# Optimization experiments

Measured on AMD Instinct MI355X. Metric: run time of the kernel, lower is better.

Reference implementation:

```python
import jax, jax.numpy as jnp
import numpy as np


def make_base_grid(D, H, W, dtype):
    # torch.affine_grid(align_corners=True) base coords: last dim is (x, y, z)
    # where x varies along W, y along H, z along D, each in [-1, 1].
    zs = jnp.linspace(-1.0, 1.0, D, dtype=dtype)
    ys = jnp.linspace(-1.0, 1.0, H, dtype=dtype)
    xs = jnp.linspace(-1.0, 1.0, W, dtype=dtype)
    gz, gy, gx = jnp.meshgrid(zs, ys, xs, indexing='ij')  # each (D,H,W)
    return jnp.stack([gx, gy, gz], axis=-1)  # (D,H,W,3)


def trilinear_sample(vol, grid):
    # vol: (C,D,H,W); grid: (D,H,W,3) normalized coords (x,y,z);
    # align_corners=True, padding_mode='zeros' (torch grid_sample defaults).
    C, D, H, W = vol.shape
    ix = (grid[..., 0] + 1.0) * 0.5 * (W - 1)
    iy = (grid[..., 1] + 1.0) * 0.5 * (H - 1)
    iz = (grid[..., 2] + 1.0) * 0.5 * (D - 1)
    ix0f, iy0f, iz0f = jnp.floor(ix), jnp.floor(iy), jnp.floor(iz)
    wx, wy, wz = ix - ix0f, iy - iy0f, iz - iz0f
    ix0, iy0, iz0 = ix0f.astype(jnp.int32), iy0f.astype(jnp.int32), iz0f.astype(jnp.int32)
    ix1, iy1, iz1 = ix0 + 1, iy0 + 1, iz0 + 1

    def corner(zi, yi, xi, w):
        valid = ((zi >= 0) & (zi < D) & (yi >= 0) & (yi < H) & (xi >= 0) & (xi < W))
        zc = jnp.clip(zi, 0, D - 1)
        yc = jnp.clip(yi, 0, H - 1)
        xc = jnp.clip(xi, 0, W - 1)
        v = vol[:, zc, yc, xc]  # (C,D,H,W)
        return v * (w * valid.astype(vol.dtype))[None]

    one = jnp.asarray(1.0, vol.dtype)
    out = (corner(iz0, iy0, ix0, (one - wz) * (one - wy) * (one - wx))
           + corner(iz0, iy0, ix1, (one - wz) * (one - wy) * wx)
           + corner(iz0, iy1, ix0, (one - wz) * wy * (one - wx))
           + corner(iz0, iy1, ix1, (one - wz) * wy * wx)
           + corner(iz1, iy0, ix0, wz * (one - wy) * (one - wx))
           + corner(iz1, iy0, ix1, wz * (one - wy) * wx)
           + corner(iz1, iy1, ix0, wz * wy * (one - wx))
           + corner(iz1, iy1, ix1, wz * wy * wx))
    return out  # (C,D,H,W)


def setup_inputs() -> dict:
    key = jax.random.key(0)
    kx, ky = jax.random.split(key)
    shape = (1, 1, 192, 192, 192)
    x = jax.random.uniform(kx, shape, dtype=jnp.float32)
    y = jax.random.uniform(ky, shape, dtype=jnp.float32)
    return {"x": x, "y": y}


def reference(x, y):
    N, C, D, H, W = x.shape
    base = make_base_grid(D, H, W, x.dtype)  # (D,H,W,3) == identity affine_grid
    xv = x[:, 0]  # (N,D,H,W), channel 0 only as in the torch code
    yv = y[:, 0]
    x_sum = jnp.sum(x)
    y_sum = jnp.sum(y)
    # weighted center of mass for each normalized coordinate (x,y,z)
    cm_x = jnp.einsum('ndhw,dhwk->k', xv, base) / x_sum  # (3,)
    cm_y = jnp.einsum('ndhw,dhwk->k', yv, base) / y_sum  # (3,)
    t = cm_x - cm_y  # translation placed in theta[:, :, 3]
    grid = base + t  # (D,H,W,3): affine_grid with identity + translation
    grid_b = jnp.broadcast_to(grid[None], (N, D, H, W, 3))
    transformed = jax.vmap(trilinear_sample)(x, grid_b)  # (N,C,D,H,W)
    return transformed, grid_b
```

## Files before the change

### kernel.cpp

```cpp
#include <hip/hip_runtime.h>
#include <math.h>

#define DD 192
#define HH 192
#define WW 192
#define NVOX (DD*HH*WW)
#define NV4  (NVOX/4)
#define RB   1024
#define RT   256

__device__ __forceinline__ float gcoord(int i, int n) {
    return -1.0f + (float)i * (2.0f / (float)(n - 1));
}

__global__ void reduce_kernel(const float* __restrict__ x,
                              const float* __restrict__ y,
                              double* __restrict__ partials) {
    double acc[8] = {0,0,0,0,0,0,0,0};
    int tid = blockIdx.x * blockDim.x + threadIdx.x;
    const float4* x4 = (const float4*)x;
    const float4* y4 = (const float4*)y;
    for (int i = tid; i < NV4; i += RB * RT) {
        float4 xv = x4[i];
        float4 yv = y4[i];
        int base = i * 4;
        int w = base % WW;
        int rem = base / WW;
        int h = rem % HH;
        int d = rem / HH;
        float gy = gcoord(h, HH);
        float gz = gcoord(d, DD);
        float xs[4] = {xv.x, xv.y, xv.z, xv.w};
        float ys[4] = {yv.x, yv.y, yv.z, yv.w};
        #pragma unroll
        for (int k = 0; k < 4; ++k) {
            float gx = gcoord(w + k, WW);
            acc[0] += (double)xs[k];
            acc[1] += (double)(xs[k] * gx);
            acc[2] += (double)(xs[k] * gy);
            acc[3] += (double)(xs[k] * gz);
            acc[4] += (double)ys[k];
            acc[5] += (double)(ys[k] * gx);
            acc[6] += (double)(ys[k] * gy);
            acc[7] += (double)(ys[k] * gz);
        }
    }
    #pragma unroll
    for (int q = 0; q < 8; ++q) {
        double v = acc[q];
        #pragma unroll
        for (int off = 32; off > 0; off >>= 1)
            v += __shfl_down(v, off, 64);
        acc[q] = v;
    }
    __shared__ double lds[4][8];
    int lane = threadIdx.x & 63;
    int wave = threadIdx.x >> 6;
    if (lane == 0) {
        #pragma unroll
        for (int q = 0; q < 8; ++q) lds[wave][q] = acc[q];
    }
    __syncthreads();
    if (threadIdx.x < 8) {
        int q = threadIdx.x;
        double s = lds[0][q] + lds[1][q] + lds[2][q] + lds[3][q];
        partials[q * RB + blockIdx.x] = s;
    }
}

__global__ void finalize_kernel(const double* __restrict__ partials,
                                float* __restrict__ tvec) {
    __shared__ double red[256];
    double sums[8];
    for (int q = 0; q < 8; ++q) {
        double s = 0.0;
        for (int i = threadIdx.x; i < RB; i += 256) s += partials[q * RB + i];
        red[threadIdx.x] = s;
        __syncthreads();
        for (int stride = 128; stride > 0; stride >>= 1) {
            if (threadIdx.x < stride) red[threadIdx.x] += red[threadIdx.x + stride];
            __syncthreads();
        }
        if (threadIdx.x == 0) sums[q] = red[0];
        __syncthreads();
    }
    if (threadIdx.x == 0) {
        double tx = sums[1] / sums[0] - sums[5] / sums[4];
        double ty = sums[2] / sums[0] - sums[6] / sums[4];
        double tz = sums[3] / sums[0] - sums[7] / sums[4];
        tvec[0] = (float)tx;
        tvec[1] = (float)ty;
        tvec[2] = (float)tz;
    }
}

__global__ void main_kernel(const float* __restrict__ x,
                            const float* __restrict__ tvec,
                            float* __restrict__ out_t,
                            float* __restrict__ out_g) {
    int idx = blockIdx.x * blockDim.x + threadIdx.x;
    if (idx >= NVOX) return;
    float tx = tvec[0], ty = tvec[1], tz = tvec[2];
    int w = idx % WW;
    int rem = idx / WW;
    int h = rem % HH;
    int d = rem / HH;
    float gx = gcoord(w, WW) + tx;
    float gy = gcoord(h, HH) + ty;
    float gz = gcoord(d, DD) + tz;
    out_g[3 * idx + 0] = gx;
    out_g[3 * idx + 1] = gy;
    out_g[3 * idx + 2] = gz;
    float ix = (gx + 1.0f) * 0.5f * (float)(WW - 1);
    float iy = (gy + 1.0f) * 0.5f * (float)(HH - 1);
    float iz = (gz + 1.0f) * 0.5f * (float)(DD - 1);
    float fx = floorf(ix), fy = floorf(iy), fz = floorf(iz);
    float wx = ix - fx, wy = iy - fy, wz = iz - fz;
    int ix0 = (int)fx, iy0 = (int)fy, iz0 = (int)fz;
    float acc = 0.0f;
    #pragma unroll
    for (int dz = 0; dz < 2; ++dz) {
        int zi = iz0 + dz;
        if ((unsigned)zi >= (unsigned)DD) continue;
        float wzz = dz ? wz : 1.0f - wz;
        #pragma unroll
        for (int dy = 0; dy < 2; ++dy) {
            int yi = iy0 + dy;
            if ((unsigned)yi >= (unsigned)HH) continue;
            float wyy = dy ? wy : 1.0f - wy;
            #pragma unroll
            for (int dx = 0; dx < 2; ++dx) {
                int xi = ix0 + dx;
                if ((unsigned)xi >= (unsigned)WW) continue;
                float wxx = dx ? wx : 1.0f - wx;
                acc += x[(zi * HH + yi) * WW + xi] * (wzz * wyy * wxx);
            }
        }
    }
    out_t[idx] = acc;
}

extern "C" void kernel_launch(void* const* d_in, const int* in_sizes, int n_in,
                              void* d_out, int out_size, void* d_ws, size_t ws_size,
                              hipStream_t stream) {
    const float* x = (const float*)d_in[0];
    const float* y = (const float*)d_in[1];
    float* out = (float*)d_out;
    float* out_t = out;
    float* out_g = out + NVOX;
    double* partials = (double*)d_ws;
    float* tvec = (float*)((char*)d_ws + 8 * RB * sizeof(double));
    reduce_kernel<<<RB, RT, 0, stream>>>(x, y, partials);
    finalize_kernel<<<1, 256, 0, stream>>>(partials, tvec);
    main_kernel<<<(NVOX + 255) / 256, 256, 0, stream>>>(x, tvec, out_t, out_g);
}
```

Measured before the change: 198.2 us.

## Precompute uniform trilinear weights and offsets; stage grid output through LDS

Since the translation is the same for every voxel, the finalize kernel now computes the integer offsets and the eight trilinear weights once. The main kernel then uses integer index arithmetic plus validity masks in place of per-voxel floor and weight math. The grid output is staged through shared memory and written as coalesced float4 stores instead of strided scalar stores. The finalize reduction switches to wave shuffles. Precomputing the weights in double could differ slightly from the per-voxel float rounding in the reference.

After: 174.7 us. -11.8%, faster.

```diff
diff --git a/kernel.cpp b/kernel.cpp
--- a/kernel.cpp
+++ b/kernel.cpp
@@ -8,6 +8,12 @@
 #define NV4  (NVOX/4)
 #define RB   1024
 #define RT   256
+
+struct Consts {
+    float tx, ty, tz;
+    float wgt[8];
+    int   dx0, dy0, dz0;
+};
 
 __device__ __forceinline__ float gcoord(int i, int n) {
     return -1.0f + (float)i * (2.0f / (float)(n - 1));
@@ -63,80 +69,101 @@
     __syncthreads();
     if (threadIdx.x < 8) {
         int q = threadIdx.x;
-        double s = lds[0][q] + lds[1][q] + lds[2][q] + lds[3][q];
-        partials[q * RB + blockIdx.x] = s;
+        partials[q * RB + blockIdx.x] = lds[0][q] + lds[1][q] + lds[2][q] + lds[3][q];
     }
 }
 
 __global__ void finalize_kernel(const double* __restrict__ partials,
-                                float* __restrict__ tvec) {
-    __shared__ double red[256];
-    double sums[8];
+                                Consts* __restrict__ cs) {
+    double s[8];
+    #pragma unroll
     for (int q = 0; q < 8; ++q) {
-        double s = 0.0;
-        for (int i = threadIdx.x; i < RB; i += 256) s += partials[q * RB + i];
-        red[threadIdx.x] = s;
-        __syncthreads();
-        for (int stride = 128; stride > 0; stride >>= 1) {
-            if (threadIdx.x < stride) red[threadIdx.x] += red[threadIdx.x + stride];
-            __syncthreads();
-        }
-        if (threadIdx.x == 0) sums[q] = red[0];
-        __syncthreads();
+        double v = 0.0;
+        for (int i = threadIdx.x; i < RB; i += 256) v += partials[q * RB + i];
+        #pragma unroll
+        for (int off = 32; off > 0; off >>= 1)
+            v += __shfl_down(v, off, 64);
+        s[q] = v;
     }
+    __shared__ double lds[4][8];
+    int lane = threadIdx.x & 63;
+    int wave = threadIdx.x >> 6;
+    if (lane == 0) {
+        #pragma unroll
+        for (int q = 0; q < 8; ++q) lds[wave][q] = s[q];
+    }
+    __syncthreads();
     if (threadIdx.x == 0) {
+        double sums[8];
+        #pragma unroll
+        for (int q = 0; q < 8; ++q)
+            sums[q] = lds[0][q] + lds[1][q] + lds[2][q] + lds[3][q];
         double tx = sums[1] / sums[0] - sums[5] / sums[4];
         double ty = sums[2] / sums[0] - sums[6] / sums[4];
         double tz = sums[3] / sums[0] - sums[7] / sums[4];
-        tvec[0] = (float)tx;
-        tvec[1] = (float)ty;
-        tvec[2] = (float)tz;
+        cs->tx = (float)tx; cs->ty = (float)ty; cs->tz = (float)tz;
+        double cx = tx * (double)(WW - 1) * 0.5;
+        double cy = ty * (double)(HH - 1) * 0.5;
+        double cz = tz * (double)(DD - 1) * 0.5;
+        double fx = floor(cx), fy = floor(cy), fz = floor(cz);
+        float wx = (float)(cx - fx), wy = (float)(cy - fy), wz = (float)(cz - fz);
+        cs->dx0 = (int)fx; cs->dy0 = (int)fy; cs->dz0 = (int)fz;
+        #pragma unroll
+        for (int k = 0; k < 8; ++k) {
+            float wzz = (k & 4) ? wz : 1.0f - wz;
+            float wyy = (k & 2) ? wy : 1.0f - wy;
+            float wxx = (k & 1) ? wx : 1.0f - wx;
+            cs->wgt[k] = wzz * wyy * wxx;
+        }
     }
 }
 
-__global__ void main_kernel(const float* __restrict__ x,
-                            const float* __restrict__ tvec,
-                            float* __restrict__ out_t,
-                            float* __restrict__ out_g) {
-    int idx = blockIdx.x * blockDim.x + threadIdx.x;
-    if (idx >= NVOX) return;
-    float tx = tvec[0], ty = tvec[1], tz = tvec[2];
+__global__ void __launch_bounds__(256) main_kernel(const float* __restrict__ x,
+                                                   const Consts* __restrict__ csp,
+                                                   float* __restrict__ out_t,
+                                                   float4* __restrict__ out_g4) {
+    __shared__ float gbuf[768];
+    const Consts c = *csp;
+    int idx = blockIdx.x * 256 + threadIdx.x;
     int w = idx % WW;
     int rem = idx / WW;
     int h = rem % HH;
     int d = rem / HH;
-    float gx = gcoord(w, WW) + tx;
-    float gy = gcoord(h, HH) + ty;
-    float gz = gcoord(d, DD) + tz;
-    out_g[3 * idx + 0] = gx;
-    out_g[3 * idx + 1] = gy;
-    out_g[3 * idx + 2] = gz;
-    float ix = (gx + 1.0f) * 0.5f * (float)(WW - 1);
-    float iy = (gy + 1.0f) * 0.5f * (float)(HH - 1);
-    float iz = (gz + 1.0f) * 0.5f * (float)(DD - 1);
-    float fx = floorf(ix), fy = floorf(iy), fz = floorf(iz);
-    float wx = ix - fx, wy = iy - fy, wz = iz - fz;
-    int ix0 = (int)fx, iy0 = (int)fy, iz0 = (int)fz;
-    float acc = 0.0f;
-    #pragma unroll
-    for (int dz = 0; dz < 2; ++dz) {
-        int zi = iz0 + dz;
-        if ((unsigned)zi >= (unsigned)DD) continue;
-        float wzz = dz ? wz : 1.0f - wz;
-        #pragma unroll
-        for (int dy = 0; dy < 2; ++dy) {
-            int yi = iy0 + dy;
-            if ((unsigned)yi >= (unsigned)HH) continue;
-            float wyy = dy ? wy : 1.0f - wy;
-            #pragma unroll
-            for (int dx = 0; dx < 2; ++dx) {
-                int xi = ix0 + dx;
-                if ((unsigned)xi >= (unsigned)WW) continue;
-                float wxx = dx ? wx : 1.0f - wx;
-                acc += x[(zi * HH + yi) * WW + xi] * (wzz * wyy * wxx);
-            }
-        }
+    float gx = gcoord(w, WW) + c.tx;
+    float gy = gcoord(h, HH) + c.ty;
+    float gz = gcoord(d, DD) + c.tz;
+    gbuf[3 * threadIdx.x + 0] = gx;
+    gbuf[3 * threadIdx.x + 1] = gy;
+    gbuf[3 * threadIdx.x + 2] = gz;
+    __syncthreads();
+    if (threadIdx.x < 192) {
+        const float4* src = (const float4*)gbuf;
+        out_g4[blockIdx.x * 192 + threadIdx.x] = src[threadIdx.x];
     }
+    int xi0 = w + c.dx0, yi0 = h + c.dy0, zi0 = d + c.dz0;
+    int xi1 = xi0 + 1,  yi1 = yi0 + 1,  zi1 = zi0 + 1;
+    int xs0 = min(max(xi0, 0), WW - 1), xs1 = min(max(xi1, 0), WW - 1);
+    int ys0 = min(max(yi0, 0), HH - 1), ys1 = min(max(yi1, 0), HH - 1);
+    int zs0 = min(max(zi0, 0), DD - 1), zs1 = min(max(zi1, 0), DD - 1);
+    float vx0 = ((unsigned)xi0 < (unsigned)WW) ? 1.0f : 0.0f;
+    float vx1 = ((unsigned)xi1 < (unsigned)WW) ? 1.0f : 0.0f;
+    float vy0 = ((unsigned)yi0 < (unsigned)HH) ? 1.0f : 0.0f;
+    float vy1 = ((unsigned)yi1 < (unsigned)HH) ? 1.0f : 0.0f;
+    float vz0 = ((unsigned)zi0 < (unsigned)DD) ? 1.0f : 0.0f;
+    float vz1 = ((unsigned)zi1 < (unsigned)DD) ? 1.0f : 0.0f;
+    int rb00 = (zs0 * HH + ys0) * WW;
+    int rb01 = (zs0 * HH + ys1) * WW;
+    int rb10 = (zs1 * HH + ys0) * WW;
+    int rb11 = (zs1 * HH + ys1) * WW;
+    float acc =
+        x[rb00 + xs0] * (c.wgt[0] * (vz0 * vy0 * vx0)) +
+        x[rb00 + xs1] * (c.wgt[1] * (vz0 * vy0 * vx1)) +
+        x[rb01 + xs0] * (c.wgt[2] * (vz0 * vy1 * vx0)) +
+        x[rb01 + xs1] * (c.wgt[3] * (vz0 * vy1 * vx1)) +
+        x[rb10 + xs0] * (c.wgt[4] * (vz1 * vy0 * vx0)) +
+        x[rb10 + xs1] * (c.wgt[5] * (vz1 * vy0 * vx1)) +
+        x[rb11 + xs0] * (c.wgt[6] * (vz1 * vy1 * vx0)) +
+        x[rb11 + xs1] * (c.wgt[7] * (vz1 * vy1 * vx1));
     out_t[idx] = acc;
 }
 
@@ -147,10 +174,10 @@
     const float* y = (const float*)d_in[1];
     float* out = (float*)d_out;
     float* out_t = out;
-    float* out_g = out + NVOX;
+    float4* out_g4 = (float4*)(out + NVOX);
     double* partials = (double*)d_ws;
-    float* tvec = (float*)((char*)d_ws + 8 * RB * sizeof(double));
+    Consts* cs = (Consts*)((char*)d_ws + 8 * RB * sizeof(double));
     reduce_kernel<<<RB, RT, 0, stream>>>(x, y, partials);
-    finalize_kernel<<<1, 256, 0, stream>>>(partials, tvec);
-    main_kernel<<<(NVOX + 255) / 256, 256, 0, stream>>>(x, tvec, out_t, out_g);
+    finalize_kernel<<<1, 256, 0, stream>>>(partials, cs);
+    main_kernel<<<NVOX / 256, 256, 0, stream>>>(x, cs, out_t, out_g4);
 }
```
